# Optimization experiments

Measured on AMD Instinct MI355X. Metric: run time of the kernel, lower is better.

Reference implementation:

```python
import jax, jax.numpy as jnp
from jax import lax
import numpy as np

DIM = 48
HEADS = 2
HIDDEN = 96  # int(dim * 2.0)
EPS_LN = 1e-5
EPS_NORM = 1e-12


def _ln(x, w, b):
    # WithBias LayerNorm over channel dim (dim=1 in NCHW == last dim in b,(hw),c)
    mu = jnp.mean(x, axis=1, keepdims=True)
    var = jnp.var(x, axis=1, keepdims=True)
    return (x - mu) / jnp.sqrt(var + EPS_LN) * w[None, :, None, None] + b[None, :, None, None]


def _conv1x1(x, w, b):
    # w: [O, C, 1, 1]
    return jnp.einsum('bchw,oc->bohw', x, w[:, :, 0, 0]) + b[None, :, None, None]


def _dwconv3(x, w, b):
    # w: [C, 1, 3, 3], groups=C
    y = lax.conv_general_dilated(x, w, (1, 1), 'SAME',
                                 feature_group_count=x.shape[1],
                                 dimension_numbers=('NCHW', 'OIHW', 'NCHW'))
    return y + b[None, :, None, None]


def _l2norm(x):
    n = jnp.sqrt(jnp.sum(x * x, axis=-1, keepdims=True))
    return x / jnp.maximum(n, EPS_NORM)


def setup_inputs() -> dict:
    key = jax.random.key(0)
    ks = jax.random.split(key, 12)
    s = 0.02
    inp = {
        'x': jax.random.normal(ks[0], (2, DIM, 64, 64), jnp.float32),
        'norm1_w': jnp.ones((DIM,), jnp.float32),
        'norm1_b': jnp.zeros((DIM,), jnp.float32),
        'qkv_w': jax.random.normal(ks[1], (DIM * 3, DIM, 1, 1), jnp.float32) * s,
        'qkv_b': jnp.zeros((DIM * 3,), jnp.float32),
        'qkvdw_w': jax.random.normal(ks[2], (DIM * 3, 1, 3, 3), jnp.float32) * s,
        'qkvdw_b': jnp.zeros((DIM * 3,), jnp.float32),
        'temperature': jnp.ones((HEADS, 1, 1), jnp.float32),
        'proj_w': jax.random.normal(ks[3], (DIM, DIM, 1, 1), jnp.float32) * s,
        'proj_b': jnp.zeros((DIM,), jnp.float32),
        'norm2_w': jnp.ones((DIM,), jnp.float32),
        'norm2_b': jnp.zeros((DIM,), jnp.float32),
        'fi_w': jax.random.normal(ks[4], (HIDDEN * 2, DIM, 1, 1), jnp.float32) * s,
        'fi_b': jnp.zeros((HIDDEN * 2,), jnp.float32),
        'fdw_w': jax.random.normal(ks[5], (HIDDEN * 2, 1, 3, 3), jnp.float32) * s,
        'fdw_b': jnp.zeros((HIDDEN * 2,), jnp.float32),
        'fo_w': jax.random.normal(ks[6], (DIM, HIDDEN, 1, 1), jnp.float32) * s,
        'fo_b': jnp.zeros((DIM,), jnp.float32),
    }
    return inp


def _block(x, norm1_w, norm1_b, qkv_w, qkv_b, qkvdw_w, qkvdw_b, temperature,
           proj_w, proj_b, norm2_w, norm2_b, fi_w, fi_b, fdw_w, fdw_b, fo_w, fo_b):
    b, c, h, w = x.shape
    n = h * w
    chead = c // HEADS
    # --- attention branch ---
    xn = _ln(x, norm1_w, norm1_b)
    qkv = _dwconv3(_conv1x1(xn, qkv_w, qkv_b), qkvdw_w, qkvdw_b)
    q, k, v = jnp.split(qkv, 3, axis=1)
    def to_heads(t):  # [b, heads*chead, h, w] -> [b, heads, n, chead]
        return t.reshape(b, HEADS, chead, n).transpose(0, 1, 3, 2)
    q, k, v = to_heads(q), to_heads(k), to_heads(v)
    q = _l2norm(q)
    k = _l2norm(k)
    attn = jnp.einsum('bhnc,bhmc->bhnm', q, k) * temperature[None]
    attn = jax.nn.softmax(attn, axis=-1)
    out = jnp.einsum('bhnm,bhmc->bhnc', attn, v)
    out = out.transpose(0, 1, 3, 2).reshape(b, c, h, w)
    x = x + _conv1x1(out, proj_w, proj_b)
    # --- ffn branch ---
    xn = _ln(x, norm2_w, norm2_b)
    y = _dwconv3(_conv1x1(xn, fi_w, fi_b), fdw_w, fdw_b)
    y1, y2 = jnp.split(y, 2, axis=1)
    y = jax.nn.gelu(y1, approximate=False) * y2
    x = x + _conv1x1(y, fo_w, fo_b)
    return x


def reference(x, norm1_w, norm1_b, qkv_w, qkv_b, qkvdw_w, qkvdw_b, temperature,
              proj_w, proj_b, norm2_w, norm2_b, fi_w, fi_b, fdw_w, fdw_b, fo_w, fo_b):
    return _block(x, norm1_w, norm1_b, qkv_w, qkv_b, qkvdw_w, qkvdw_b, temperature,
                  proj_w, proj_b, norm2_w, norm2_b, fi_w, fi_b, fdw_w, fdw_b, fo_w, fo_b)
```

## Files before the change

### kernel.cpp

```cpp
#include <hip/hip_runtime.h>
#include <hip/hip_bf16.h>
#include <math.h>

#define NPIX 4096
#define DIMC 48
#define NB 2
#define SPLIT 4

typedef __attribute__((ext_vector_type(8))) short short8;
typedef __attribute__((ext_vector_type(4))) short short4s;
typedef __attribute__((ext_vector_type(4))) float floatx4;

static __device__ inline short f2bf(float f) {
    union { float f; unsigned u; } v; v.f = f;
    unsigned r = (v.u + 0x7FFFu + ((v.u >> 16) & 1u)) >> 16;
    return (short)r;
}
static __device__ inline float bf2f(short s) {
    union { unsigned u; float f; } v;
    v.u = ((unsigned)(unsigned short)s) << 16;
    return v.f;
}

__global__ void k_prepw(const float* __restrict__ qkvw, const float* __restrict__ fiw,
                        const float* __restrict__ fow, const float* __restrict__ projw,
                        short* __restrict__ qkvwbf, short* __restrict__ fiwbf,
                        short* __restrict__ fowbf, short* __restrict__ projwbf) {
    int idx = blockIdx.x * 256 + threadIdx.x;
    if (idx < 144 * 64) {
        int o = idx >> 6, c = idx & 63;
        qkvwbf[idx] = (c < 48) ? f2bf(qkvw[o * 48 + c]) : (short)0;
        return;
    }
    idx -= 144 * 64;
    if (idx < 192 * 64) {
        int o = idx >> 6, c = idx & 63;
        fiwbf[idx] = (c < 48) ? f2bf(fiw[o * 48 + c]) : (short)0;
        return;
    }
    idx -= 192 * 64;
    if (idx < 48 * 96) {
        fowbf[idx] = f2bf(fow[idx]);
        return;
    }
    idx -= 48 * 96;
    if (idx < 48 * 64) {
        int o = idx >> 6, c = idx & 63;
        projwbf[idx] = (c < 48) ? f2bf(projw[o * 48 + c]) : (short)0;
    }
}

__global__ __launch_bounds__(256) void k_ln_conv_mfma(
    const float* __restrict__ xin, const float* __restrict__ lw, const float* __restrict__ lb,
    const short* __restrict__ wbf, const float* __restrict__ cb,
    short* __restrict__ outbf, int OC)
{
    int px0 = blockIdx.x * 32;
    int b = blockIdx.y;
    int t = threadIdx.x;
    int w = t >> 6, lane = t & 63, l15 = lane & 15, quad = lane >> 4;

    __shared__ float psum[8][32], psq[8][32];
    __shared__ float muS[32], rsS[32];
    __shared__ short xnbf[32][72];

    int px = t & 31, g = t >> 5;
    *(unsigned*)&xnbf[px][48 + g * 2] = 0u;

    float v[6];
    float s = 0.f, sq = 0.f;
#pragma unroll
    for (int i = 0; i < 6; i++) {
        v[i] = xin[((size_t)b * 48 + g * 6 + i) * (size_t)NPIX + px0 + px];
        s += v[i]; sq += v[i] * v[i];
    }
    psum[g][px] = s; psq[g][px] = sq;
    __syncthreads();
    if (t < 32) {
        float ss = 0.f, qq = 0.f;
#pragma unroll
        for (int i = 0; i < 8; i++) { ss += psum[i][t]; qq += psq[i][t]; }
        float mu = ss * (1.f / 48.f);
        float var = qq * (1.f / 48.f) - mu * mu;
        muS[t] = mu; rsS[t] = rsqrtf(var + 1e-5f);
    }
    __syncthreads();
    {
        float mu = muS[px], rs = rsS[px];
#pragma unroll
        for (int i = 0; i < 6; i++) {
            int c = g * 6 + i;
            xnbf[px][c] = f2bf((v[i] - mu) * rs * lw[c] + lb[c]);
        }
    }
    __syncthreads();
    floatx4 zf = {0.f, 0.f, 0.f, 0.f};
    int oct = OC >> 4;
    int njobs = 2 * oct;
    for (int job = w; job < njobs; job += 4) {
        int pt = job / oct, ot = job % oct;
        short8 a0 = *(const short8*)&xnbf[pt * 16 + l15][quad * 8];
        short8 a1 = *(const short8*)&xnbf[pt * 16 + l15][32 + quad * 8];
        const short* wb = wbf + (ot * 16 + l15) * 64;
        short8 b0 = *(const short8*)(wb + quad * 8);
        short8 b1 = *(const short8*)(wb + 32 + quad * 8);
        floatx4 c = __builtin_amdgcn_mfma_f32_16x16x32_bf16(a0, b0, zf, 0, 0, 0);
        c = __builtin_amdgcn_mfma_f32_16x16x32_bf16(a1, b1, c, 0, 0, 0);
        int oc = ot * 16 + l15;
        float bi = cb[oc];
        short4s st;
#pragma unroll
        for (int r = 0; r < 4; r++) st[r] = f2bf(c[r] + bi);
        *(short4s*)(outbf + ((size_t)b * OC + oc) * (size_t)NPIX + px0 + pt * 16 + quad * 4) = st;
    }
}

__global__ __launch_bounds__(256) void k_dw3heads(
    const short* __restrict__ qkv_pre, const float* __restrict__ dww,
    const float* __restrict__ dwb, const float* __restrict__ temp,
    short* __restrict__ Qbf, short* __restrict__ Kbf, short* __restrict__ Vbf)
{
    int px0 = blockIdx.x * 16;
    int y = blockIdx.y, b = blockIdx.z;
    int t = threadIdx.x;
    int wx0 = px0 - 8; if (wx0 < 0) wx0 = 0; if (wx0 > 32) wx0 = 32;
    int xoff = px0 - wx0;

    __shared__ short stage[3][144][40];
    __shared__ float q2[16][148];

    for (int seg = t; seg < 3 * 144 * 4; seg += 256) {
        int q = seg & 3, idx = seg >> 2;
        int c = idx % 144, r = idx / 144;
        int yy = y + r - 1;
        short8 ld = {};
        if ((unsigned)yy < 64u)
            ld = *(const short8*)(qkv_pre + (size_t)(b * 144 + c) * NPIX + yy * 64 + wx0 + q * 8);
        *(short8*)&stage[r][c][q * 8] = ld;
    }
    __syncthreads();
    int px = t & 15, g = t >> 4;
    {
        int sbase = xoff + px;
        for (int i = 0; i < 9; i++) {
            int c = g * 9 + i;
            const float* wp = dww + c * 9;
            float acc = dwb[c];
#pragma unroll
            for (int dy = 0; dy < 3; dy++) {
#pragma unroll
                for (int dx = -1; dx <= 1; dx++) {
                    int si = sbase + dx;
                    if ((unsigned)si < 32u)
                        acc += bf2f(stage[dy][c][si]) * wp[dy * 3 + dx + 1];
                }
            }
            q2[px][c] = acc;
        }
    }
    __syncthreads();
    if (t < 32) {
        int hpx = t & 15, h = t >> 4;
        int n = y * 64 + px0 + hpx;
        int bh = b * 2 + h;
        float q[24], k[24], vv[24]; float sqs = 0.f, sks = 0.f;
#pragma unroll
        for (int c = 0; c < 24; c++) {
            q[c] = q2[hpx][h * 24 + c];       sqs += q[c] * q[c];
            k[c] = q2[hpx][48 + h * 24 + c];  sks += k[c] * k[c];
            vv[c] = q2[hpx][96 + h * 24 + c];
        }
        float rq = temp[h] / fmaxf(sqrtf(sqs), 1e-12f);
        float rk = 1.f / fmaxf(sqrtf(sks), 1e-12f);
        short qs[32], ks[32];
#pragma unroll
        for (int c = 0; c < 24; c++) { qs[c] = f2bf(q[c] * rq); ks[c] = f2bf(k[c] * rk); }
#pragma unroll
        for (int c = 24; c < 32; c++) { qs[c] = 0; ks[c] = 0; }
        size_t ro = ((size_t)bh * NPIX + n) * 32;
#pragma unroll
        for (int i = 0; i < 4; i++) {
            short8 a, bb;
#pragma unroll
            for (int j = 0; j < 8; j++) { a[j] = qs[i * 8 + j]; bb[j] = ks[i * 8 + j]; }
            *(short8*)(Qbf + ro + i * 8) = a;
            *(short8*)(Kbf + ro + i * 8) = bb;
        }
        int r5 = n & 31;
        int vcol = (n & ~31) + ((r5 & 15) * 2 + (r5 >> 4));
#pragma unroll
        for (int c = 0; c < 24; c++)
            Vbf[((size_t)bh * 32 + c) * NPIX + vcol] = f2bf(vv[c]);
#pragma unroll
        for (int c = 24; c < 32; c++)
            Vbf[((size_t)bh * 32 + c) * NPIX + vcol] = 0;
    }
}

__global__ __launch_bounds__(256) void k_attn_mfma(const short* __restrict__ Qbf,
                                                   const short* __restrict__ Kbf,
                                                   const short* __restrict__ Vbf,
                                                   float* __restrict__ Opart,
                                                   float* __restrict__ lpart) {
    int qt = blockIdx.x, s = blockIdx.y, bh = blockIdx.z;
    int t = threadIdx.x;
    int w = t >> 6, lane = t & 63, l15 = lane & 15, quad = lane >> 4;

    __shared__ short tileK[2][64][40];
    __shared__ short tileV[2][32][72];
    __shared__ short P[4][16][72];

    int qrow0 = qt * 64 + w * 16;
    short8 aq = *(const short8*)(Qbf + ((size_t)bh * NPIX + qrow0 + l15) * 32 + quad * 8);

    int krow = t >> 2, kseg = t & 3;
    int vch = t >> 3, vseg = t & 7;
    const short* srcK = Kbf + ((size_t)bh * NPIX + krow) * 32 + kseg * 8;
    const short* srcV = Vbf + ((size_t)(bh * 32 + vch)) * NPIX + vseg * 8;

    int key0 = s * (NPIX / SPLIT);
    *(short8*)&tileK[0][krow][kseg * 8] = *(const short8*)(srcK + (size_t)key0 * 32);
    *(short8*)&tileV[0][vch][vseg * 8]  = *(const short8*)(srcV + key0);

    floatx4 zf = {0.f, 0.f, 0.f, 0.f};
    floatx4 o0 = zf, o1 = zf;
    float ls[4] = {0.f, 0.f, 0.f, 0.f};

    const int NKT = (NPIX / SPLIT) / 64;
    for (int kt = 0; kt < NKT; kt++) {
        __syncthreads();
        int cur = kt & 1;
        short8 ldK = {}, ldV = {};
        if (kt < NKT - 1) {
            int kabs = key0 + (kt + 1) * 64;
            ldK = *(const short8*)(srcK + (size_t)kabs * 32);
            ldV = *(const short8*)(srcV + kabs);
        }
        short8 kb0 = *(const short8*)&tileK[cur][l15][quad * 8];
        short8 kb1 = *(const short8*)&tileK[cur][16 + l15][quad * 8];
        short8 kb2 = *(const short8*)&tileK[cur][32 + l15][quad * 8];
        short8 kb3 = *(const short8*)&tileK[cur][48 + l15][quad * 8];
        floatx4 s0 = __builtin_amdgcn_mfma_f32_16x16x32_bf16(aq, kb0, zf, 0, 0, 0);
        floatx4 s1 = __builtin_amdgcn_mfma_f32_16x16x32_bf16(aq, kb1, zf, 0, 0, 0);
        floatx4 s2 = __builtin_amdgcn_mfma_f32_16x16x32_bf16(aq, kb2, zf, 0, 0, 0);
        floatx4 s3 = __builtin_amdgcn_mfma_f32_16x16x32_bf16(aq, kb3, zf, 0, 0, 0);
#pragma unroll
        for (int r = 0; r < 4; r++) {
            float p0 = __expf(s0[r]);
            float p1 = __expf(s1[r]);
            float p2 = __expf(s2[r]);
            float p3 = __expf(s3[r]);
            ls[r] += (p0 + p1) + (p2 + p3);
            __hip_bfloat162 pk01 = __float22bfloat162_rn(make_float2(p0, p1));
            __hip_bfloat162 pk23 = __float22bfloat162_rn(make_float2(p2, p3));
            *(unsigned*)&P[w][quad * 4 + r][l15 * 2]      = *(unsigned*)&pk01;
            *(unsigned*)&P[w][quad * 4 + r][32 + l15 * 2] = *(unsigned*)&pk23;
        }
        short8 ap0 = *(const short8*)&P[w][l15][quad * 8];
        short8 ap1 = *(const short8*)&P[w][l15][32 + quad * 8];
        short8 vb00 = *(const short8*)&tileV[cur][l15][quad * 8];
        short8 vb01 = *(const short8*)&tileV[cur][l15][32 + quad * 8];
        short8 vb10 = *(const short8*)&tileV[cur][16 + l15][quad * 8];
        short8 vb11 = *(const short8*)&tileV[cur][16 + l15][32 + quad * 8];
        o0 = __builtin_amdgcn_mfma_f32_16x16x32_bf16(ap0, vb00, o0, 0, 0, 0);
        o0 = __builtin_amdgcn_mfma_f32_16x16x32_bf16(ap1, vb01, o0, 0, 0, 0);
        o1 = __builtin_amdgcn_mfma_f32_16x16x32_bf16(ap0, vb10, o1, 0, 0, 0);
        o1 = __builtin_amdgcn_mfma_f32_16x16x32_bf16(ap1, vb11, o1, 0, 0, 0);
        if (kt < NKT - 1) {
            *(short8*)&tileK[1 - cur][krow][kseg * 8] = ldK;
            *(short8*)&tileV[1 - cur][vch][vseg * 8]  = ldV;
        }
    }
#pragma unroll
    for (int m = 1; m < 16; m <<= 1) {
#pragma unroll
        for (int r = 0; r < 4; r++) ls[r] += __shfl_xor(ls[r], m, 64);
    }
#pragma unroll
    for (int r = 0; r < 4; r++) {
        int n = qrow0 + quad * 4 + r;
        size_t base2 = (size_t)(bh * SPLIT + s) * 32;
        Opart[(base2 + l15) * NPIX + n] = o0[r];
        Opart[(base2 + 16 + l15) * NPIX + n] = o1[r];
        if (l15 == 0) lpart[((size_t)(bh * SPLIT + s)) * NPIX + n] = ls[r];
    }
}

__global__ __launch_bounds__(256) void k_projlnfi(
    const float* __restrict__ x, const float* __restrict__ Opart,
    const float* __restrict__ lpart, const short* __restrict__ projwbf,
    const float* __restrict__ projb,
    const float* __restrict__ n2w, const float* __restrict__ n2b,
    const short* __restrict__ fiwbf, const float* __restrict__ fib,
    float* __restrict__ x1, short* __restrict__ fp_pre)
{
    int px0 = blockIdx.x * 32;
    int b = blockIdx.y;
    int t = threadIdx.x;
    int w = t >> 6, lane = t & 63, l15 = lane & 15, quad = lane >> 4;

    __shared__ __align__(16) short Ash[32][72];
    __shared__ float rlsh[2][32];
    __shared__ float x1sh[32][53];
    __shared__ float psum[8][32], psq[8][32];
    __shared__ float muS[32], rsS[32];
    __shared__ short xnbf[32][72];

    if (t < 64) {
        int h = t >> 5, px = t & 31;
        float l = 0.f;
#pragma unroll
        for (int s = 0; s < SPLIT; s++)
            l += lpart[((size_t)((b * 2 + h) * SPLIT + s)) * NPIX + px0 + px];
        rlsh[h][px] = 1.f / l;
    }
    {
        int px = t & 31, j = t >> 5;
        *(unsigned*)&Ash[px][48 + j * 2] = 0u;
        *(unsigned*)&xnbf[px][48 + j * 2] = 0u;
    }
    __syncthreads();
#pragma unroll
    for (int pi = 0; pi < 6; pi++) {
        int idx = pi * 256 + t;
        int px = idx & 31, c = idx >> 5;
        int h = c / 24, ch = c % 24;
        float acc = 0.f;
#pragma unroll
        for (int s = 0; s < SPLIT; s++)
            acc += Opart[(((size_t)((b * 2 + h) * SPLIT + s)) * 32 + ch) * NPIX + px0 + px];
        Ash[px][c] = f2bf(acc * rlsh[h][px]);
    }
    __syncthreads();
    floatx4 zf = {0.f, 0.f, 0.f, 0.f};
    for (int job = w; job < 6; job += 4) {
        int pt = job / 3, ot = job % 3;
        short8 a0 = *(const short8*)&Ash[pt * 16 + l15][quad * 8];
        short8 a1 = *(const short8*)&Ash[pt * 16 + l15][32 + quad * 8];
        const short* wb = projwbf + (ot * 16 + l15) * 64;
        short8 b0 = *(const short8*)(wb + quad * 8);
        short8 b1 = *(const short8*)(wb + 32 + quad * 8);
        floatx4 c = __builtin_amdgcn_mfma_f32_16x16x32_bf16(a0, b0, zf, 0, 0, 0);
        c = __builtin_amdgcn_mfma_f32_16x16x32_bf16(a1, b1, c, 0, 0, 0);
        int oc = ot * 16 + l15;
        float bi = projb[oc];
#pragma unroll
        for (int r = 0; r < 4; r++) {
            int px = pt * 16 + quad * 4 + r;
            size_t idx = ((size_t)b * 48 + oc) * NPIX + px0 + px;
            float val = x[idx] + c[r] + bi;
            x1[idx] = val;
            x1sh[px][oc] = val;
        }
    }
    __syncthreads();
    int px = t & 31, g = t >> 5;
    float v[6];
    float s = 0.f, sq = 0.f;
#pragma unroll
    for (int i = 0; i < 6; i++) {
        v[i] = x1sh[px][g * 6 + i];
        s += v[i]; sq += v[i] * v[i];
    }
    psum[g][px] = s; psq[g][px] = sq;
    __syncthreads();
    if (t < 32) {
        float ss = 0.f, qq = 0.f;
#pragma unroll
        for (int i = 0; i < 8; i++) { ss += psum[i][t]; qq += psq[i][t]; }
        float mu = ss * (1.f / 48.f);
        float var = qq * (1.f / 48.f) - mu * mu;
        muS[t] = mu; rsS[t] = rsqrtf(var + 1e-5f);
    }
    __syncthreads();
    {
        float mu = muS[px], rs = rsS[px];
#pragma unroll
        for (int i = 0; i < 6; i++) {
            int c = g * 6 + i;
            xnbf[px][c] = f2bf((v[i] - mu) * rs * n2w[c] + n2b[c]);
        }
    }
    __syncthreads();
    for (int job = w; job < 24; job += 4) {
        int pt = job / 12, ot = job % 12;
        short8 a0 = *(const short8*)&xnbf[pt * 16 + l15][quad * 8];
        short8 a1 = *(const short8*)&xnbf[pt * 16 + l15][32 + quad * 8];
        const short* wb = fiwbf + (ot * 16 + l15) * 64;
        short8 b0 = *(const short8*)(wb + quad * 8);
        short8 b1 = *(const short8*)(wb + 32 + quad * 8);
        floatx4 c = __builtin_amdgcn_mfma_f32_16x16x32_bf16(a0, b0, zf, 0, 0, 0);
        c = __builtin_amdgcn_mfma_f32_16x16x32_bf16(a1, b1, c, 0, 0, 0);
        int oc = ot * 16 + l15;
        float bi = fib[oc];
        short4s st;
#pragma unroll
        for (int r = 0; r < 4; r++) st[r] = f2bf(c[r] + bi);
        *(short4s*)(fp_pre + ((size_t)b * 192 + oc) * (size_t)NPIX + px0 + pt * 16 + quad * 4) = st;
    }
}

__global__ __launch_bounds__(256) void k_dwgatefo(
    const short* __restrict__ fp_pre, const float* __restrict__ fdww,
    const float* __restrict__ fdwb, const short* __restrict__ fowbf,
    const float* __restrict__ fob, const float* __restrict__ x1,
    float* __restrict__ out)
{
    int px0 = blockIdx.x * 16;
    int y = blockIdx.y, b = blockIdx.z;
    int t = threadIdx.x;
    int w = t >> 6, lane = t & 63, l15 = lane & 15, quad = lane >> 4;
    int wx0 = px0 - 8; if (wx0 < 0) wx0 = 0; if (wx0 > 32) wx0 = 32;
    int xoff = px0 - wx0;

    __shared__ short stage[3][192][40];
    __shared__ short yv[16][104];

    for (int seg = t; seg < 3 * 192 * 4; seg += 256) {
        int q = seg & 3, idx = seg >> 2;
        int c = idx % 192, r = idx / 192;
        int yy = y + r - 1;
        short8 ld = {};
        if ((unsigned)yy < 64u)
            ld = *(const short8*)(fp_pre + (size_t)(b * 192 + c) * NPIX + yy * 64 + wx0 + q * 8);
        *(short8*)&stage[r][c][q * 8] = ld;
    }
    __syncthreads();
    int px = t & 15, g = t >> 4;
    {
        int sbase = xoff + px;
        for (int i = 0; i < 6; i++) {
            int c = g * 6 + i;
            const float* wp  = fdww + c * 9;
            const float* wp2 = fdww + (c + 96) * 9;
            float a  = fdwb[c];
            float g2 = fdwb[c + 96];
#pragma unroll
            for (int dy = 0; dy < 3; dy++) {
#pragma unroll
                for (int dx = -1; dx <= 1; dx++) {
                    int si = sbase + dx;
                    if ((unsigned)si < 32u) {
                        a  += bf2f(stage[dy][c][si])      * wp[dy * 3 + dx + 1];
                        g2 += bf2f(stage[dy][c + 96][si]) * wp2[dy * 3 + dx + 1];
                    }
                }
            }
            float ge = 0.5f * a * (1.f + erff(a * 0.70710678118654752f));
            yv[px][c] = f2bf(ge * g2);
        }
    }
    __syncthreads();
    if (w < 3) {
        floatx4 c = {0.f, 0.f, 0.f, 0.f};
#pragma unroll
        for (int k = 0; k < 3; k++) {
            short8 a = *(const short8*)&yv[l15][k * 32 + quad * 8];
            short8 bb = *(const short8*)(fowbf + (w * 16 + l15) * 96 + k * 32 + quad * 8);
            c = __builtin_amdgcn_mfma_f32_16x16x32_bf16(a, bb, c, 0, 0, 0);
        }
        int oc = w * 16 + l15;
        float bi = fob[oc];
#pragma unroll
        for (int r = 0; r < 4; r++) {
            int n = y * 64 + px0 + quad * 4 + r;
            size_t idx = ((size_t)b * 48 + oc) * NPIX + n;
            out[idx] = x1[idx] + c[r] + bi;
        }
    }
}

extern "C" void kernel_launch(void* const* d_in, const int* in_sizes, int n_in,
                              void* d_out, int out_size, void* d_ws, size_t ws_size,
                              hipStream_t stream) {
    const float* x       = (const float*)d_in[0];
    const float* n1w     = (const float*)d_in[1];
    const float* n1b     = (const float*)d_in[2];
    const float* qkv_w   = (const float*)d_in[3];
    const float* qkv_b   = (const float*)d_in[4];
    const float* qkvdw_w = (const float*)d_in[5];
    const float* qkvdw_b = (const float*)d_in[6];
    const float* temp    = (const float*)d_in[7];
    const float* proj_w  = (const float*)d_in[8];
    const float* proj_b  = (const float*)d_in[9];
    const float* n2w     = (const float*)d_in[10];
    const float* n2b     = (const float*)d_in[11];
    const float* fi_w    = (const float*)d_in[12];
    const float* fi_b    = (const float*)d_in[13];
    const float* fdw_w   = (const float*)d_in[14];
    const float* fdw_b   = (const float*)d_in[15];
    const float* fo_w    = (const float*)d_in[16];
    const float* fo_b    = (const float*)d_in[17];

    float* ws = (float*)d_ws;
    short* qkv_pre = (short*)ws;
    short* fp_pre  = (short*)(ws + 589824);
    short* Qbf     = (short*)(ws + 1376256);
    short* Kbf     = (short*)(ws + 1638400);
    short* Vbf     = (short*)(ws + 1900544);
    float* Opart   = ws + 2162688;
    float* lpart   = ws + 4259840;
    float* x1      = ws + 4325376;
    short* qkvwbf  = (short*)(ws + 4718592);
    short* fiwbf   = qkvwbf + 9216;
    short* fowbf   = fiwbf + 12288;
    short* projwbf = fowbf + 4608;

    {
        int total = 144 * 64 + 192 * 64 + 48 * 96 + 48 * 64;
        k_prepw<<<(total + 255) / 256, 256, 0, stream>>>(qkv_w, fi_w, fo_w, proj_w,
                                                         qkvwbf, fiwbf, fowbf, projwbf);
    }
    {
        dim3 g(128, NB);
        k_ln_conv_mfma<<<g, 256, 0, stream>>>(x, n1w, n1b, qkvwbf, qkv_b, qkv_pre, 144);
    }
    {
        dim3 g(4, 64, NB);
        k_dw3heads<<<g, 256, 0, stream>>>(qkv_pre, qkvdw_w, qkvdw_b, temp, Qbf, Kbf, Vbf);
    }
    {
        dim3 g(64, SPLIT, 4);
        k_attn_mfma<<<g, 256, 0, stream>>>(Qbf, Kbf, Vbf, Opart, lpart);
    }
    {
        dim3 g(128, NB);
        k_projlnfi<<<g, 256, 0, stream>>>(x, Opart, lpart, projwbf, proj_b,
                                          n2w, n2b, fiwbf, fi_b, x1, fp_pre);
    }
    {
        dim3 g(4, 64, NB);
        k_dwgatefo<<<g, 256, 0, stream>>>(fp_pre, fdw_w, fdw_b, fowbf, fo_b, x1,
                                          (float*)d_out);
    }
}
```

Baseline: 150.3 us.

## Transpose attention MFMAs so probabilities stay in registers, dropping LDS round-trip

The QK^T product is computed transposed (K as the A operand, Q as B), so each lane's exp outputs already sit in the layout the PV MFMA needs as its B operand. The shared-memory P buffer and its write/read round-trip are removed. The V global layout permutation is changed to match the new key ordering, and the row-sum reduction needs only two cross-lane shuffles. This lowers LDS traffic and the register/LDS pressure in the inner loop, at the cost of a trickier coupled layout between the prep and attention kernels.

New measurement: 148.9 us, median of 2. About the same (-1.0%).

```diff
diff --git a/kernel.cpp b/kernel.cpp
--- a/kernel.cpp
+++ b/kernel.cpp
@@ -20,6 +20,10 @@
     union { unsigned u; float f; } v;
     v.u = ((unsigned)(unsigned short)s) << 16;
     return v.f;
+}
+static __device__ inline unsigned pk2(float a, float b) {
+    __hip_bfloat162 pk = __float22bfloat162_rn(make_float2(a, b));
+    return *(unsigned*)&pk;
 }
 
 __global__ void k_prepw(const float* __restrict__ qkvw, const float* __restrict__ fiw,
@@ -187,7 +191,9 @@
             *(short8*)(Kbf + ro + i * 8) = bb;
         }
         int r5 = n & 31;
-        int vcol = (n & ~31) + ((r5 & 15) * 2 + (r5 >> 4));
+        int pos = (r5 < 16) ? ((r5 >> 2) * 8 + (r5 & 3))
+                            : (((r5 & 15) >> 2) * 8 + (r5 & 3) + 4);
+        int vcol = (n & ~31) + pos;
 #pragma unroll
         for (int c = 0; c < 24; c++)
             Vbf[((size_t)bh * 32 + c) * NPIX + vcol] = f2bf(vv[c]);
@@ -208,10 +214,9 @@
 
     __shared__ short tileK[2][64][40];
     __shared__ short tileV[2][32][72];
-    __shared__ short P[4][16][72];
 
     int qrow0 = qt * 64 + w * 16;
-    short8 aq = *(const short8*)(Qbf + ((size_t)bh * NPIX + qrow0 + l15) * 32 + quad * 8);
+    short8 bq = *(const short8*)(Qbf + ((size_t)bh * NPIX + qrow0 + l15) * 32 + quad * 8);
 
     int krow = t >> 2, kseg = t & 3;
     int vch = t >> 3, vseg = t & 7;
@@ -224,7 +229,7 @@
 
     floatx4 zf = {0.f, 0.f, 0.f, 0.f};
     floatx4 o0 = zf, o1 = zf;
-    float ls[4] = {0.f, 0.f, 0.f, 0.f};
+    float ls = 0.f;
 
     const int NKT = (NPIX / SPLIT) / 64;
     for (int kt = 0; kt < NKT; kt++) {
@@ -236,54 +241,53 @@
             ldK = *(const short8*)(srcK + (size_t)kabs * 32);
             ldV = *(const short8*)(srcV + kabs);
         }
-        short8 kb0 = *(const short8*)&tileK[cur][l15][quad * 8];
-        short8 kb1 = *(const short8*)&tileK[cur][16 + l15][quad * 8];
-        short8 kb2 = *(const short8*)&tileK[cur][32 + l15][quad * 8];
-        short8 kb3 = *(const short8*)&tileK[cur][48 + l15][quad * 8];
-        floatx4 s0 = __builtin_amdgcn_mfma_f32_16x16x32_bf16(aq, kb0, zf, 0, 0, 0);
-        floatx4 s1 = __builtin_amdgcn_mfma_f32_16x16x32_bf16(aq, kb1, zf, 0, 0, 0);
-        floatx4 s2 = __builtin_amdgcn_mfma_f32_16x16x32_bf16(aq, kb2, zf, 0, 0, 0);
-        floatx4 s3 = __builtin_amdgcn_mfma_f32_16x16x32_bf16(aq, kb3, zf, 0, 0, 0);
+        short8 ka0 = *(const short8*)&tileK[cur][l15][quad * 8];
+        short8 ka1 = *(const short8*)&tileK[cur][16 + l15][quad * 8];
+        short8 ka2 = *(const short8*)&tileK[cur][32 + l15][quad * 8];
+        short8 ka3 = *(const short8*)&tileK[cur][48 + l15][quad * 8];
+        floatx4 s0 = __builtin_amdgcn_mfma_f32_16x16x32_bf16(ka0, bq, zf, 0, 0, 0);
+        floatx4 s1 = __builtin_amdgcn_mfma_f32_16x16x32_bf16(ka1, bq, zf, 0, 0, 0);
+        floatx4 s2 = __builtin_amdgcn_mfma_f32_16x16x32_bf16(ka2, bq, zf, 0, 0, 0);
+        floatx4 s3 = __builtin_amdgcn_mfma_f32_16x16x32_bf16(ka3, bq, zf, 0, 0, 0);
+        float e0[4], e1[4], e2[4], e3[4];
 #pragma unroll
         for (int r = 0; r < 4; r++) {
-            float p0 = __expf(s0[r]);
-            float p1 = __expf(s1[r]);
-            float p2 = __expf(s2[r]);
-            float p3 = __expf(s3[r]);
-            ls[r] += (p0 + p1) + (p2 + p3);
-            __hip_bfloat162 pk01 = __float22bfloat162_rn(make_float2(p0, p1));
-            __hip_bfloat162 pk23 = __float22bfloat162_rn(make_float2(p2, p3));
-            *(unsigned*)&P[w][quad * 4 + r][l15 * 2]      = *(unsigned*)&pk01;
-            *(unsigned*)&P[w][quad * 4 + r][32 + l15 * 2] = *(unsigned*)&pk23;
-        }
-        short8 ap0 = *(const short8*)&P[w][l15][quad * 8];
-        short8 ap1 = *(const short8*)&P[w][l15][32 + quad * 8];
-        short8 vb00 = *(const short8*)&tileV[cur][l15][quad * 8];
-        short8 vb01 = *(const short8*)&tileV[cur][l15][32 + quad * 8];
-        short8 vb10 = *(const short8*)&tileV[cur][16 + l15][quad * 8];
-        short8 vb11 = *(const short8*)&tileV[cur][16 + l15][32 + quad * 8];
-        o0 = __builtin_amdgcn_mfma_f32_16x16x32_bf16(ap0, vb00, o0, 0, 0, 0);
-        o0 = __builtin_amdgcn_mfma_f32_16x16x32_bf16(ap1, vb01, o0, 0, 0, 0);
-        o1 = __builtin_amdgcn_mfma_f32_16x16x32_bf16(ap0, vb10, o1, 0, 0, 0);
-        o1 = __builtin_amdgcn_mfma_f32_16x16x32_bf16(ap1, vb11, o1, 0, 0, 0);
+            e0[r] = __expf(s0[r]); e1[r] = __expf(s1[r]);
+            e2[r] = __expf(s2[r]); e3[r] = __expf(s3[r]);
+            ls += (e0[r] + e1[r]) + (e2[r] + e3[r]);
+        }
+        short8 p01, p23;
+        {
+            unsigned* u01 = (unsigned*)&p01;
+            unsigned* u23 = (unsigned*)&p23;
+            u01[0] = pk2(e0[0], e0[1]); u01[1] = pk2(e0[2], e0[3]);
+            u01[2] = pk2(e1[0], e1[1]); u01[3] = pk2(e1[2], e1[3]);
+            u23[0] = pk2(e2[0], e2[1]); u23[1] = pk2(e2[2], e2[3]);
+            u23[2] = pk2(e3[0], e3[1]); u23[3] = pk2(e3[2], e3[3]);
+        }
+        short8 va00 = *(const short8*)&tileV[cur][l15][quad * 8];
+        short8 va01 = *(const short8*)&tileV[cur][l15][32 + quad * 8];
+        short8 va10 = *(const short8*)&tileV[cur][16 + l15][quad * 8];
+        short8 va11 = *(const short8*)&tileV[cur][16 + l15][32 + quad * 8];
+        o0 = __builtin_amdgcn_mfma_f32_16x16x32_bf16(va00, p01, o0, 0, 0, 0);
+        o0 = __builtin_amdgcn_mfma_f32_16x16x32_bf16(va01, p23, o0, 0, 0, 0);
+        o1 = __builtin_amdgcn_mfma_f32_16x16x32_bf16(va10, p01, o1, 0, 0, 0);
+        o1 = __builtin_amdgcn_mfma_f32_16x16x32_bf16(va11, p23, o1, 0, 0, 0);
         if (kt < NKT - 1) {
             *(short8*)&tileK[1 - cur][krow][kseg * 8] = ldK;
             *(short8*)&tileV[1 - cur][vch][vseg * 8]  = ldV;
         }
     }
-#pragma unroll
-    for (int m = 1; m < 16; m <<= 1) {
-#pragma unroll
-        for (int r = 0; r < 4; r++) ls[r] += __shfl_xor(ls[r], m, 64);
-    }
+    ls += __shfl_xor(ls, 16, 64);
+    ls += __shfl_xor(ls, 32, 64);
+    int n = qrow0 + l15;
+    size_t base2 = (size_t)(bh * SPLIT + s) * 32;
 #pragma unroll
     for (int r = 0; r < 4; r++) {
-        int n = qrow0 + quad * 4 + r;
-        size_t base2 = (size_t)(bh * SPLIT + s) * 32;
-        Opart[(base2 + l15) * NPIX + n] = o0[r];
-        Opart[(base2 + 16 + l15) * NPIX + n] = o1[r];
-        if (l15 == 0) lpart[((size_t)(bh * SPLIT + s)) * NPIX + n] = ls[r];
-    }
+        Opart[(base2 + quad * 4 + r) * NPIX + n] = o0[r];
+        Opart[(base2 + 16 + quad * 4 + r) * NPIX + n] = o1[r];
+    }
+    if (quad == 0) lpart[((size_t)(bh * SPLIT + s)) * NPIX + n] = ls;
 }
 
 __global__ __launch_bounds__(256) void k_projlnfi(
```
